# Kernel tuning notes

Hardware: AMD Instinct MI355X
Metric: run time of the kernel (lower is better)

The kernel has to match this reference:

```python
import jax, jax.numpy as jnp
import numpy as np

B, T, FEA, H, OUT, L = 40, 20, 200, 1024, 1095, 12


def setup_inputs() -> dict:
    key = jax.random.key(0)
    ks = jax.random.split(key, 8)

    def init(k, shape, fan_in):
        return jax.random.normal(k, shape, jnp.float32) * (1.0 / np.sqrt(fan_in))

    return {
        "x": jax.random.normal(ks[0], (B, T, FEA), jnp.float32),
        "hidden": jnp.zeros((L, B, H), jnp.float32),  # initial SRU cell state c0 per layer
        "W1": init(ks[1], (FEA, H), FEA),
        "b1": jnp.zeros((H,), jnp.float32),
        "sru_W": init(ks[2], (L, H, 3 * H), H),   # per layer: [x_tilde | f-gate | r-gate]
        "sru_b": jnp.zeros((L, 2 * H), jnp.float32),  # per layer: [b_f | b_r]
        "W3": init(ks[3], (H, H), H),
        "b3": jnp.zeros((H,), jnp.float32),
        "W4": init(ks[4], (H, OUT), H),
        "b4": jnp.zeros((OUT,), jnp.float32),
    }


def _sru_layer(x, c0, W, b):
    # x: [t, b, h]; SRU (Lei et al. 2017) with use_tanh=True and highway on x
    U = jnp.einsum('tbh,hk->tbk', x, W)          # [t, b, 3h]
    x_tilde, uf, ur = jnp.split(U, 3, axis=-1)
    bf, br = jnp.split(b, 2)
    f = jax.nn.sigmoid(uf + bf)                  # forget gate
    r = jax.nn.sigmoid(ur + br)                  # reset/highway gate

    def step(c, ins):
        ft, xt = ins
        c = ft * c + (1.0 - ft) * xt
        return c, c

    c_last, cs = jax.lax.scan(step, c0, (f, x_tilde))
    h = r * jnp.tanh(cs) + (1.0 - r) * x
    return h, c_last


def reference(x, hidden, W1, b1, sru_W, sru_b, W3, b3, W4, b4):
    b, t, _ = x.shape
    # Dense_layer1 (dropout is identity at inference)
    h = jnp.dot(x.reshape(b * t, -1), W1) + b1
    h = h.reshape(b, t, H).transpose(1, 0, 2)    # [t, b, H] (time-major for SRU)
    c_finals = []
    for l in range(sru_W.shape[0]):
        h, c_l = _sru_layer(h, hidden[l], sru_W[l], sru_b[l])
        c_finals.append(c_l)
    hidden_after = jnp.stack(c_finals)           # [L, b, H]
    h = h.transpose(1, 0, 2).reshape(b * t, H)
    h = jax.nn.relu(jnp.dot(h, W3) + b3)
    out = jnp.dot(h, W4) + b4                    # [b*t, OUT]
    return out, hidden_after
```

## Files before the change

### kernel.cpp

```cpp
#include <hip/hip_runtime.h>
#include <hip/hip_bf16.h>
#include <math.h>

typedef __bf16 bf16_t;
typedef __bf16 bf16x8 __attribute__((ext_vector_type(8)));
typedef float f32x4 __attribute__((ext_vector_type(4)));
typedef unsigned short u16;

#define NB   40
#define NT   20
#define FEA  200
#define HD   1024
#define NOUT 1095
#define NL   12
#define M_ROWS 800
#define UPITCH 196

#define FBUF 36864
#define GBUF 24576

__global__ __launch_bounds__(256)
void transpose_convert(const float* __restrict__ src, bf16_t* __restrict__ dst,
                       int srcK, int srcN, int Kp, int Np)
{
    __shared__ u16 tile[64 * 66];
    const int t = threadIdx.x;
    src += (size_t)blockIdx.z * srcK * srcN;
    dst += (size_t)blockIdx.z * Np * Kp;
    const int n0 = blockIdx.x << 6, k0 = blockIdx.y << 6;
    {
        const int nl = t & 63, kb = (t >> 6) << 4;
        const int gn = n0 + nl;
        #pragma unroll
        for (int j = 0; j < 16; j++) {
            const int gk = k0 + kb + j;
            float v = (gk < srcK && gn < srcN) ? src[(size_t)gk * srcN + gn] : 0.f;
            bf16_t b = (bf16_t)v;
            tile[nl * 66 + kb + j] = *(const u16*)&b;
        }
    }
    __syncthreads();
    {
        const int nl = t >> 2, kg = (t & 3) << 4;
        const unsigned* tp = (const unsigned*)tile;
        const int dw = nl * 33 + (kg >> 1);
        uint4 v0, v1;
        v0.x = tp[dw+0]; v0.y = tp[dw+1]; v0.z = tp[dw+2]; v0.w = tp[dw+3];
        v1.x = tp[dw+4]; v1.y = tp[dw+5]; v1.z = tp[dw+6]; v1.w = tp[dw+7];
        bf16_t* dp = dst + (size_t)(n0 + nl) * Kp + k0 + kg;
        *(uint4*)dp = v0;
        *(uint4*)(dp + 8) = v1;
    }
}

__global__ __launch_bounds__(256)
void convert_pad_x(const float* __restrict__ src, bf16_t* __restrict__ dst)
{
    const int m = blockIdx.x, k = threadIdx.x;
    dst[m * 256 + k] = (bf16_t)((k < FEA) ? src[(size_t)m * FEA + k] : 0.f);
}

template<bool OUT_F32, bool RELU>
__global__ __launch_bounds__(256)
void gemm_tiled(const bf16_t* __restrict__ A, const bf16_t* __restrict__ Bt,
                const float* __restrict__ bias, void* __restrict__ C,
                int M, int Nstore, int Ks)
{
    extern __shared__ char lds[];
    const int tid = threadIdx.x;
    const int w = tid >> 6, lane = tid & 63, quad = lane >> 4, l16 = lane & 15;
    const int n0 = blockIdx.x << 6;
    const int m0 = blockIdx.y << 7;
    const int wr = w >> 1, wc = w & 1;

    const int lrow  = lane >> 3;
    const int gslot = ((lane & 7) ^ lrow) << 3;
    const bf16_t* aSrc[4];
    const bf16_t* bSrc[2];
    #pragma unroll
    for (int i = 0; i < 4; i++) {
        int r = m0 + (w * 4 + i) * 8 + lrow;
        if (r > M - 1) r = M - 1;
        aSrc[i] = A + (size_t)r * Ks + gslot;
    }
    #pragma unroll
    for (int i = 0; i < 2; i++)
        bSrc[i] = Bt + (size_t)(n0 + (w * 2 + i) * 8 + lrow) * Ks + gslot;

    f32x4 acc[4][2];
    #pragma unroll
    for (int m = 0; m < 4; m++)
        #pragma unroll
        for (int n = 0; n < 2; n++) acc[m][n] = (f32x4){0.f, 0.f, 0.f, 0.f};

    const int nkt = Ks >> 6;

    #define STAGE(kt) do {                                                     \
        const int _k0 = (kt) << 6;                                             \
        char* _b = lds + ((kt) & 3) * GBUF;                                    \
        _Pragma("unroll")                                                      \
        for (int _i = 0; _i < 4; _i++)                                         \
            __builtin_amdgcn_global_load_lds(                                  \
                (const __attribute__((address_space(1))) void*)(aSrc[_i] + _k0),\
                (__attribute__((address_space(3))) void*)(_b + (w * 4 + _i) * 1024), \
                16, 0, 0);                                                     \
        _Pragma("unroll")                                                      \
        for (int _i = 0; _i < 2; _i++)                                         \
            __builtin_amdgcn_global_load_lds(                                  \
                (const __attribute__((address_space(1))) void*)(bSrc[_i] + _k0),\
                (__attribute__((address_space(3))) void*)(_b + 16384 + (w * 2 + _i) * 1024), \
                16, 0, 0);                                                     \
    } while (0)

    STAGE(0);
    if (nkt > 1) STAGE(1);

    for (int kt = 0; kt < nkt; kt++) {
        if (kt + 2 < nkt) STAGE(kt + 2);
        const int rem = nkt - 1 - kt;
        if (rem >= 2)      asm volatile("s_waitcnt vmcnt(12)" ::: "memory");
        else if (rem == 1) asm volatile("s_waitcnt vmcnt(6)"  ::: "memory");
        else               asm volatile("s_waitcnt vmcnt(0)"  ::: "memory");
        __builtin_amdgcn_s_barrier();

        const char* ab = lds + (kt & 3) * GBUF;
        #pragma unroll
        for (int kk = 0; kk < 2; kk++) {
            const int ts = (kk << 2) + quad;
            bf16x8 a[4], b[2];
            #pragma unroll
            for (int m = 0; m < 4; m++) {
                const int r = wr * 64 + m * 16 + l16;
                a[m] = *(const bf16x8*)(ab + r * 128 + ((ts ^ (r & 7)) << 4));
            }
            #pragma unroll
            for (int n = 0; n < 2; n++) {
                const int r = wc * 32 + n * 16 + l16;
                b[n] = *(const bf16x8*)(ab + 16384 + r * 128 + ((ts ^ (r & 7)) << 4));
            }
            #pragma unroll
            for (int m = 0; m < 4; m++)
                #pragma unroll
                for (int n = 0; n < 2; n++)
                    acc[m][n] = __builtin_amdgcn_mfma_f32_16x16x32_bf16(a[m], b[n], acc[m][n], 0, 0, 0);
        }
    }
    #undef STAGE

    #pragma unroll
    for (int n = 0; n < 2; n++) {
        const int col = n0 + wc * 32 + n * 16 + l16;
        if (col >= Nstore) continue;
        const float bv = bias ? bias[col] : 0.f;
        #pragma unroll
        for (int m = 0; m < 4; m++) {
            #pragma unroll
            for (int i = 0; i < 4; i++) {
                const int mg = m0 + wr * 64 + m * 16 + quad * 4 + i;
                if (mg < M) {
                    float v = acc[m][n][i] + bv;
                    if (RELU) v = v > 0.f ? v : 0.f;
                    if (OUT_F32) ((float*)C)[(size_t)mg * Nstore + col] = v;
                    else         ((bf16_t*)C)[(size_t)mg * Nstore + col] = (bf16_t)v;
                }
            }
        }
    }
}

__global__ __launch_bounds__(256)
void sru_layer_fused(const bf16_t* __restrict__ hin, bf16_t* __restrict__ hout,
                     const bf16_t* __restrict__ Wt, const float* __restrict__ c0,
                     const float* __restrict__ bvec, float* __restrict__ cout)
{
    extern __shared__ char lds_raw[];
    const int tid = threadIdx.x;
    const int w = tid >> 6, lane = tid & 63, quad = lane >> 4, l16 = lane & 15;
    const int n0 = blockIdx.x << 6;
    const int m0 = blockIdx.y * 80;

    const int lrow  = lane >> 3;
    const int gslot = ((lane & 7) ^ lrow) << 3;

    const bf16_t* aSrc[3];
    #pragma unroll
    for (int i = 0; i < 3; i++) {
        int r = (w * 3 + i) * 8 + lrow;
        if (r > 79) r = 79;
        aSrc[i] = hin + (size_t)(m0 + r) * HD + gslot;
    }
    const bf16_t* bSrc[6];
    #pragma unroll
    for (int i = 0; i < 6; i++) {
        const int r = (w * 6 + i) * 8 + lrow;
        bSrc[i] = Wt + (size_t)((r >> 6) * HD + n0 + (r & 63)) * HD + gslot;
    }

    f32x4 acc[5][3];
    #pragma unroll
    for (int m = 0; m < 5; m++)
        #pragma unroll
        for (int n = 0; n < 3; n++) acc[m][n] = (f32x4){0.f, 0.f, 0.f, 0.f};

    #define STAGEF(kt) do {                                                    \
        const int _k0 = (kt) << 6;                                             \
        char* _b = lds_raw + ((kt) & 3) * FBUF;                                \
        _Pragma("unroll")                                                      \
        for (int _i = 0; _i < 3; _i++)                                         \
            __builtin_amdgcn_global_load_lds(                                  \
                (const __attribute__((address_space(1))) void*)(aSrc[_i] + _k0), \
                (__attribute__((address_space(3))) void*)(_b + (w * 3 + _i) * 1024), \
                16, 0, 0);                                                     \
        _Pragma("unroll")                                                      \
        for (int _i = 0; _i < 6; _i++)                                         \
            __builtin_amdgcn_global_load_lds(                                  \
                (const __attribute__((address_space(1))) void*)(bSrc[_i] + _k0), \
                (__attribute__((address_space(3))) void*)(_b + 12288 + (w * 6 + _i) * 1024), \
                16, 0, 0);                                                     \
    } while (0)

    STAGEF(0);
    STAGEF(1);

    for (int kt = 0; kt < 16; kt++) {
        if (kt + 2 < 16) STAGEF(kt + 2);
        const int rem = 15 - kt;
        if (rem >= 2)      asm volatile("s_waitcnt vmcnt(18)" ::: "memory");
        else if (rem == 1) asm volatile("s_waitcnt vmcnt(9)"  ::: "memory");
        else               asm volatile("s_waitcnt vmcnt(0)"  ::: "memory");
        __builtin_amdgcn_s_barrier();

        const char* ab = lds_raw + (kt & 3) * FBUF;
        const char* bb = ab + 12288;
        #pragma unroll
        for (int kk = 0; kk < 2; kk++) {
            const int ts = (kk << 2) + quad;
            bf16x8 a[5], b[3];
            #pragma unroll
            for (int m = 0; m < 5; m++) {
                const int r = m * 16 + l16;
                a[m] = *(const bf16x8*)(ab + r * 128 + ((ts ^ (r & 7)) << 4));
            }
            #pragma unroll
            for (int n = 0; n < 3; n++) {
                const int r = (w * 3 + n) * 16 + l16;
                b[n] = *(const bf16x8*)(bb + r * 128 + ((ts ^ (r & 7)) << 4));
            }
            #pragma unroll
            for (int m = 0; m < 5; m++)
                #pragma unroll
                for (int n = 0; n < 3; n++)
                    acc[m][n] = __builtin_amdgcn_mfma_f32_16x16x32_bf16(a[m], b[n], acc[m][n], 0, 0, 0);
        }
    }
    #undef STAGEF

    float* Ul = (float*)lds_raw;
    #pragma unroll
    for (int m = 0; m < 5; m++)
        #pragma unroll
        for (int n = 0; n < 3; n++) {
            const int col = (w * 3 + n) * 16 + l16;
            #pragma unroll
            for (int i = 0; i < 4; i++)
                Ul[(m * 16 + quad * 4 + i) * UPITCH + col] = acc[m][n][i];
        }
    __syncthreads();

    const int bl = tid >> 6, nn = tid & 63, bg = blockIdx.y * 4 + bl;
    float c = c0[(size_t)bg * HD + n0 + nn];
    const float bfb = bvec[n0 + nn], brb = bvec[HD + n0 + nn];
    for (int t = 0; t < NT; t++) {
        const float* u = &Ul[(bl * NT + t) * UPITCH];
        const float xt = u[nn];
        const float uf = u[64 + nn];
        const float ur = u[128 + nn];
        const float f = 1.f / (1.f + __expf(-(uf + bfb)));
        const float r = 1.f / (1.f + __expf(-(ur + brb)));
        c = f * c + (1.f - f) * xt;
        const size_t gi = (size_t)(bg * NT + t) * HD + n0 + nn;
        const float hp = (float)hin[gi];
        hout[gi] = (bf16_t)(r * tanhf(c) + (1.f - r) * hp);
    }
    cout[(size_t)bg * HD + n0 + nn] = c;
}

extern "C" void kernel_launch(void* const* d_in, const int* in_sizes, int n_in,
                              void* d_out, int out_size, void* d_ws, size_t ws_size,
                              hipStream_t stream)
{
    const float* x      = (const float*)d_in[0];
    const float* hidden = (const float*)d_in[1];
    const float* W1     = (const float*)d_in[2];
    const float* b1     = (const float*)d_in[3];
    const float* sruW   = (const float*)d_in[4];
    const float* srub   = (const float*)d_in[5];
    const float* W3     = (const float*)d_in[6];
    const float* b3     = (const float*)d_in[7];
    const float* W4     = (const float*)d_in[8];
    const float* b4     = (const float*)d_in[9];

    float* out     = (float*)d_out;
    float* hid_out = out + (size_t)M_ROWS * NOUT;

    bf16_t* h0 = (bf16_t*)d_out;

    hipFuncSetAttribute((const void*)sru_layer_fused,
                        hipFuncAttributeMaxDynamicSharedMemorySize, 4 * FBUF);
    hipFuncSetAttribute((const void*)gemm_tiled<false, false>,
                        hipFuncAttributeMaxDynamicSharedMemorySize, 4 * GBUF);
    hipFuncSetAttribute((const void*)gemm_tiled<false, true>,
                        hipFuncAttributeMaxDynamicSharedMemorySize, 4 * GBUF);
    hipFuncSetAttribute((const void*)gemm_tiled<true, false>,
                        hipFuncAttributeMaxDynamicSharedMemorySize, 4 * GBUF);

    char* ws = (char*)d_ws;
    const size_t SZ_WT  = (size_t)NL * 3 * HD * HD * 2;
    const size_t SZ_W1  = (size_t)HD * 256 * 2;
    const size_t SZ_W3  = (size_t)HD * HD * 2;
    const size_t SZ_W4  = (size_t)1152 * HD * 2;
    const size_t SZ_XB  = (size_t)M_ROWS * 256 * 2;
    const size_t SZ_H   = (size_t)M_ROWS * HD * 2;
    const size_t SLOT   = (size_t)3 * HD * HD * 2;
    const size_t FAST_NEED = SZ_WT + SZ_W1 + SZ_W3 + SZ_W4 + SZ_XB + 2 * SZ_H;
    const bool fast = ws_size >= FAST_NEED;

    const dim3 blk(256);
    const int GY = (M_ROWS + 127) >> 7;

    if (fast) {
        bf16_t* wt  = (bf16_t*)ws;
        bf16_t* w1t = (bf16_t*)(ws + SZ_WT);
        bf16_t* w3t = (bf16_t*)(ws + SZ_WT + SZ_W1);
        bf16_t* w4t = (bf16_t*)(ws + SZ_WT + SZ_W1 + SZ_W3);
        bf16_t* xb  = (bf16_t*)(ws + SZ_WT + SZ_W1 + SZ_W3 + SZ_W4);
        bf16_t* h1  = (bf16_t*)(ws + SZ_WT + SZ_W1 + SZ_W3 + SZ_W4 + SZ_XB);
        bf16_t* g   = (bf16_t*)(ws + SZ_WT + SZ_W1 + SZ_W3 + SZ_W4 + SZ_XB + SZ_H);

        convert_pad_x<<<M_ROWS, blk, 0, stream>>>(x, xb);
        transpose_convert<<<dim3(16, 4, 1),  blk, 0, stream>>>(W1,   w1t, FEA, HD,    256, HD);
        transpose_convert<<<dim3(48, 16, NL), blk, 0, stream>>>(sruW, wt,  HD,  3*HD, HD,  3*HD);
        transpose_convert<<<dim3(16, 16, 1), blk, 0, stream>>>(W3,   w3t, HD,  HD,   HD,  HD);
        transpose_convert<<<dim3(18, 16, 1), blk, 0, stream>>>(W4,   w4t, HD,  NOUT, HD,  1152);

        gemm_tiled<false, false><<<dim3(16, GY), blk, 4 * GBUF, stream>>>(xb, w1t, b1, h0, M_ROWS, HD, 256);

        for (int l = 0; l < NL; l++) {
            const bf16_t* hi = (l & 1) ? h1 : h0;
            bf16_t*       ho = (l & 1) ? h0 : h1;
            sru_layer_fused<<<dim3(16, 10), blk, 4 * FBUF, stream>>>(
                hi, ho, wt + (size_t)l * 3 * HD * HD,
                hidden + (size_t)l * NB * HD, srub + (size_t)l * 2 * HD,
                hid_out + (size_t)l * NB * HD);
        }
        gemm_tiled<false, true><<<dim3(16, GY), blk, 4 * GBUF, stream>>>(h0, w3t, b3, g, M_ROWS, HD, HD);
        gemm_tiled<true, false><<<dim3(18, GY), blk, 4 * GBUF, stream>>>(g, w4t, b4, out, M_ROWS, NOUT, HD);
    } else {
        bf16_t* slot = (bf16_t*)ws;
        bf16_t* xb   = (bf16_t*)(ws + SLOT);
        bf16_t* h1   = (bf16_t*)(ws + SLOT + SZ_XB);
        bf16_t* g    = (bf16_t*)(ws + SLOT + SZ_XB + SZ_H);

        convert_pad_x<<<M_ROWS, blk, 0, stream>>>(x, xb);
        transpose_convert<<<dim3(16, 4, 1), blk, 0, stream>>>(W1, slot, FEA, HD, 256, HD);
        gemm_tiled<false, false><<<dim3(16, GY), blk, 4 * GBUF, stream>>>(xb, slot, b1, h0, M_ROWS, HD, 256);

        for (int l = 0; l < NL; l++) {
            transpose_convert<<<dim3(48, 16, 1), blk, 0, stream>>>(
                sruW + (size_t)l * HD * 3 * HD, slot, HD, 3*HD, HD, 3*HD);
            const bf16_t* hi = (l & 1) ? h1 : h0;
            bf16_t*       ho = (l & 1) ? h0 : h1;
            sru_layer_fused<<<dim3(16, 10), blk, 4 * FBUF, stream>>>(
                hi, ho, slot,
                hidden + (size_t)l * NB * HD, srub + (size_t)l * 2 * HD,
                hid_out + (size_t)l * NB * HD);
        }
        transpose_convert<<<dim3(16, 16, 1), blk, 0, stream>>>(W3, slot, HD, HD, HD, HD);
        gemm_tiled<false, true><<<dim3(16, GY), blk, 4 * GBUF, stream>>>(h0, slot, b3, g, M_ROWS, HD, HD);
        transpose_convert<<<dim3(18, 16, 1), blk, 0, stream>>>(W4, slot, HD, NOUT, HD, 1152);
        gemm_tiled<true, false><<<dim3(18, GY), blk, 4 * GBUF, stream>>>(g, slot, b4, out, M_ROWS, NOUT, HD);
    }
}
```

Measured before the change: 544.5 us.

## Double SRU block row tile to 160 with 8 waves and triple-buffered LDS

The fused SRU layer kernel now uses 512 threads and covers 160 rows per block, so each weight tile loaded into LDS is reused by two row halves. This halves the number of blocks per layer and the redundant weight traffic. The pipeline moves from four to three LDS buffers, with the prefetch issued after the MFMA work, and tanhf is replaced by an exp-based formula. The catch is fewer blocks (80) to fill the GPU, more LDS per block, and a slightly different tanh numerically.

```diff
diff --git a/kernel.cpp b/kernel.cpp
--- a/kernel.cpp
+++ b/kernel.cpp
@@ -16,7 +16,7 @@
 #define M_ROWS 800
 #define UPITCH 196
 
-#define FBUF 36864
+#define FBUF 49152
 #define GBUF 24576
 
 __global__ __launch_bounds__(256)
@@ -168,7 +168,7 @@
     }
 }
 
-__global__ __launch_bounds__(256)
+__global__ __launch_bounds__(512)
 void sru_layer_fused(const bf16_t* __restrict__ hin, bf16_t* __restrict__ hout,
                      const bf16_t* __restrict__ Wt, const float* __restrict__ c0,
                      const float* __restrict__ bvec, float* __restrict__ cout)
@@ -176,8 +176,9 @@
     extern __shared__ char lds_raw[];
     const int tid = threadIdx.x;
     const int w = tid >> 6, lane = tid & 63, quad = lane >> 4, l16 = lane & 15;
+    const int rh = w >> 2, wq = w & 3;
     const int n0 = blockIdx.x << 6;
-    const int m0 = blockIdx.y * 80;
+    const int m0 = blockIdx.y * 160;
 
     const int lrow  = lane >> 3;
     const int gslot = ((lane & 7) ^ lrow) << 3;
@@ -186,14 +187,14 @@
     #pragma unroll
     for (int i = 0; i < 3; i++) {
         int r = (w * 3 + i) * 8 + lrow;
-        if (r > 79) r = 79;
+        if (r > 159) r = 159;
         aSrc[i] = hin + (size_t)(m0 + r) * HD + gslot;
     }
-    const bf16_t* bSrc[6];
-    #pragma unroll
-    for (int i = 0; i < 6; i++) {
-        const int r = (w * 6 + i) * 8 + lrow;
-        bSrc[i] = Wt + (size_t)((r >> 6) * HD + n0 + (r & 63)) * HD + gslot;
+    const bf16_t* bSrc[3];
+    #pragma unroll
+    for (int i = 0; i < 3; i++) {
+        const int rb = (w * 3 + i) * 8 + lrow;
+        bSrc[i] = Wt + (size_t)((rb >> 6) * HD + n0 + (rb & 63)) * HD + gslot;
     }
 
     f32x4 acc[5][3];
@@ -204,7 +205,7 @@
 
     #define STAGEF(kt) do {                                                    \
         const int _k0 = (kt) << 6;                                             \
-        char* _b = lds_raw + ((kt) & 3) * FBUF;                                \
+        char* _b = lds_raw + ((kt) % 3) * FBUF;                                \
         _Pragma("unroll")                                                      \
         for (int _i = 0; _i < 3; _i++)                                         \
             __builtin_amdgcn_global_load_lds(                                  \
@@ -212,10 +213,10 @@
                 (__attribute__((address_space(3))) void*)(_b + (w * 3 + _i) * 1024), \
                 16, 0, 0);                                                     \
         _Pragma("unroll")                                                      \
-        for (int _i = 0; _i < 6; _i++)                                         \
+        for (int _i = 0; _i < 3; _i++)                                         \
             __builtin_amdgcn_global_load_lds(                                  \
                 (const __attribute__((address_space(1))) void*)(bSrc[_i] + _k0), \
-                (__attribute__((address_space(3))) void*)(_b + 12288 + (w * 6 + _i) * 1024), \
+                (__attribute__((address_space(3))) void*)(_b + 24576 + (w * 3 + _i) * 1024), \
                 16, 0, 0);                                                     \
     } while (0)
 
@@ -223,28 +224,25 @@
     STAGEF(1);
 
     for (int kt = 0; kt < 16; kt++) {
-        if (kt + 2 < 16) STAGEF(kt + 2);
-        const int rem = 15 - kt;
-        if (rem >= 2)      asm volatile("s_waitcnt vmcnt(18)" ::: "memory");
-        else if (rem == 1) asm volatile("s_waitcnt vmcnt(9)"  ::: "memory");
-        else               asm volatile("s_waitcnt vmcnt(0)"  ::: "memory");
+        if (kt < 15) asm volatile("s_waitcnt vmcnt(6)" ::: "memory");
+        else         asm volatile("s_waitcnt vmcnt(0)" ::: "memory");
         __builtin_amdgcn_s_barrier();
 
-        const char* ab = lds_raw + (kt & 3) * FBUF;
-        const char* bb = ab + 12288;
+        const char* ab = lds_raw + (kt % 3) * FBUF;
+        const char* bb = ab + 24576;
         #pragma unroll
         for (int kk = 0; kk < 2; kk++) {
             const int ts = (kk << 2) + quad;
             bf16x8 a[5], b[3];
             #pragma unroll
             for (int m = 0; m < 5; m++) {
-                const int r = m * 16 + l16;
+                const int r = rh * 80 + m * 16 + l16;
                 a[m] = *(const bf16x8*)(ab + r * 128 + ((ts ^ (r & 7)) << 4));
             }
             #pragma unroll
             for (int n = 0; n < 3; n++) {
-                const int r = (w * 3 + n) * 16 + l16;
-                b[n] = *(const bf16x8*)(bb + r * 128 + ((ts ^ (r & 7)) << 4));
+                const int rb = (wq * 3 + n) * 16 + l16;
+                b[n] = *(const bf16x8*)(bb + rb * 128 + ((ts ^ (rb & 7)) << 4));
             }
             #pragma unroll
             for (int m = 0; m < 5; m++)
@@ -252,24 +250,28 @@
                 for (int n = 0; n < 3; n++)
                     acc[m][n] = __builtin_amdgcn_mfma_f32_16x16x32_bf16(a[m], b[n], acc[m][n], 0, 0, 0);
         }
+        if (kt + 2 < 16) STAGEF(kt + 2);
     }
     #undef STAGEF
 
+    __syncthreads();
+
     float* Ul = (float*)lds_raw;
     #pragma unroll
     for (int m = 0; m < 5; m++)
         #pragma unroll
         for (int n = 0; n < 3; n++) {
-            const int col = (w * 3 + n) * 16 + l16;
+            const int col = (wq * 3 + n) * 16 + l16;
             #pragma unroll
             for (int i = 0; i < 4; i++)
-                Ul[(m * 16 + quad * 4 + i) * UPITCH + col] = acc[m][n][i];
+                Ul[(rh * 80 + m * 16 + quad * 4 + i) * UPITCH + col] = acc[m][n][i];
         }
     __syncthreads();
 
-    const int bl = tid >> 6, nn = tid & 63, bg = blockIdx.y * 4 + bl;
+    const int bl = tid >> 6, nn = tid & 63, bg = blockIdx.y * 8 + bl;
     float c = c0[(size_t)bg * HD + n0 + nn];
     const float bfb = bvec[n0 + nn], brb = bvec[HD + n0 + nn];
+    #pragma unroll
     for (int t = 0; t < NT; t++) {
         const float* u = &Ul[(bl * NT + t) * UPITCH];
         const float xt = u[nn];
@@ -278,9 +280,12 @@
         const float f = 1.f / (1.f + __expf(-(uf + bfb)));
         const float r = 1.f / (1.f + __expf(-(ur + brb)));
         c = f * c + (1.f - f) * xt;
+        const float e  = __expf(-2.f * fabsf(c));
+        float th = (1.f - e) / (1.f + e);
+        th = (c < 0.f) ? -th : th;
         const size_t gi = (size_t)(bg * NT + t) * HD + n0 + nn;
         const float hp = (float)hin[gi];
-        hout[gi] = (bf16_t)(r * tanhf(c) + (1.f - r) * hp);
+        hout[gi] = (bf16_t)(r * th + (1.f - r) * hp);
     }
     cout[(size_t)bg * HD + n0 + nn] = c;
 }
@@ -306,7 +311,7 @@
     bf16_t* h0 = (bf16_t*)d_out;
 
     hipFuncSetAttribute((const void*)sru_layer_fused,
-                        hipFuncAttributeMaxDynamicSharedMemorySize, 4 * FBUF);
+                        hipFuncAttributeMaxDynamicSharedMemorySize, 3 * FBUF);
     hipFuncSetAttribute((const void*)gemm_tiled<false, false>,
                         hipFuncAttributeMaxDynamicSharedMemorySize, 4 * GBUF);
     hipFuncSetAttribute((const void*)gemm_tiled<false, true>,
@@ -326,6 +331,7 @@
     const bool fast = ws_size >= FAST_NEED;
 
     const dim3 blk(256);
+    const dim3 blkf(512);
     const int GY = (M_ROWS + 127) >> 7;
 
     if (fast) {
@@ -348,7 +354,7 @@
         for (int l = 0; l < NL; l++) {
             const bf16_t* hi = (l & 1) ? h1 : h0;
             bf16_t*       ho = (l & 1) ? h0 : h1;
-            sru_layer_fused<<<dim3(16, 10), blk, 4 * FBUF, stream>>>(
+            sru_layer_fused<<<dim3(16, 5), blkf, 3 * FBUF, stream>>>(
                 hi, ho, wt + (size_t)l * 3 * HD * HD,
                 hidden + (size_t)l * NB * HD, srub + (size_t)l * 2 * HD,
                 hid_out + (size_t)l * NB * HD);
@@ -370,7 +376,7 @@
                 sruW + (size_t)l * HD * 3 * HD, slot, HD, 3*HD, HD, 3*HD);
             const bf16_t* hi = (l & 1) ? h1 : h0;
             bf16_t*       ho = (l & 1) ? h0 : h1;
-            sru_layer_fused<<<dim3(16, 10), blk, 4 * FBUF, stream>>>(
+            sru_layer_fused<<<dim3(16, 5), blkf, 3 * FBUF, stream>>>(
                 hi, ho, slot,
                 hidden + (size_t)l * NB * HD, srub + (size_t)l * 2 * HD,
                 hid_out + (size_t)l * NB * HD);
```

New measurement: 556.1 us. 1.02x slower.
